# Kernel tuning notes

Hardware: AMD Instinct MI355X
Metric: run time of the kernel (lower is better)

Reference implementation:

```python
import jax, jax.numpy as jnp
import numpy as np

# dims derived from init_kwargs
B, C, T, F = 16, 2, 16, 256
TP, FP = 4, 4            # time/freq patch
MF = F // FP             # 64 freq tokens
TIC = T // TP            # 4 time tokens per chunk
S = MF * TIC             # 256 tokens per chunk
CTX = 3
LEFT = S * CTX           # 768 cached tokens
MT = TIC * (CTX + 1)     # 16 max time positions
D, H, G = 512, 8, 4      # d_model, q heads, kv groups
HD = D // H              # 64
R = H // G               # 2 q-heads per kv group
L = 4                    # layers
FFH = 4 * D
EPS = 1e-5


def _ln(x, g, b):
    m = jnp.mean(x, -1, keepdims=True)
    v = jnp.mean((x - m) ** 2, -1, keepdims=True)
    return (x - m) * jax.lax.rsqrt(v + EPS) * g + b


def setup_inputs() -> dict:
    key = jax.random.key(0)
    ks = iter(jax.random.split(key, 20))
    rn = lambda shape, s=0.05: jax.random.normal(next(ks), shape, jnp.float32) * s
    return {
        "x": rn((B, C, T, F), 1.0),
        "cache_k": rn((L, B, G, LEFT, HD), 1.0),
        "cache_v": rn((L, B, G, LEFT, HD), 1.0),
        "in_W": rn((TP * FP * C, D)), "in_b": jnp.zeros((D,)),
        "ln1_g": jnp.ones((L, D)), "ln1_b": jnp.zeros((L, D)),
        "Wq": rn((L, D, D)), "bq": jnp.zeros((L, D)),
        "Wk": rn((L, D, G * HD)), "bk": jnp.zeros((L, G * HD)),
        "Wv": rn((L, D, G * HD)), "bv": jnp.zeros((L, G * HD)),
        "Wo": rn((L, D, D)), "bo": jnp.zeros((L, D)),
        "rel_time": rn((L, 2 * MT - 1, H)), "rel_freq": rn((L, 2 * MF - 1, H)),
        "res_a": jnp.ones((L,)),
        "ln2_g": jnp.ones((L, D)), "ln2_b": jnp.zeros((L, D)),
        "W1": rn((L, D, FFH)), "b1": jnp.zeros((L, FFH)),
        "W3": rn((L, D, FFH)), "b3": jnp.zeros((L, FFH)),
        "W2": rn((L, FFH, D)), "b2": jnp.zeros((L, D)),
        "res_f": jnp.ones((L,)),
        "out_W": rn((D, TP * FP * C)), "out_b": jnp.zeros((TP * FP * C,)),
    }


def reference(x, cache_k, cache_v, in_W, in_b, ln1_g, ln1_b, Wq, bq, Wk, bk, Wv, bv,
              Wo, bo, rel_time, rel_freq, res_a, ln2_g, ln2_b, W1, b1, W3, b3, W2, b2,
              res_f, out_W, out_b):
    # patchify: (B,C,T,F) -> (B, S, TP*FP*C), token order time-major / freq inner
    h = jnp.transpose(x, (0, 2, 3, 1)).reshape(B, TIC, TP, MF, FP, C)
    h = jnp.transpose(h, (0, 1, 3, 2, 4, 5)).reshape(B, S, TP * FP * C)
    h = h @ in_W + in_b  # (B,S,D)

    # 2D relative position indices (identical each layer)
    K = LEFT + S
    q_idx = jnp.arange(S)
    k_idx = jnp.arange(K)
    qt = LEFT // MF + q_idx // MF  # query time = cache time offset + local time
    qf = q_idx % MF
    kt = k_idx // MF
    kf = k_idx % MF
    dt = qt[:, None] - kt[None, :] + (MT - 1)  # (S,K) in [0, 2*MT-2]
    df = qf[:, None] - kf[None, :] + (MF - 1)  # (S,K) in [0, 2*MF-2]
    scale = 1.0 / np.sqrt(HD).astype(np.float32)

    new_ck, new_cv = [], []
    for l in range(L):
        # --- streaming GQA attention with 2D rel-pos and KV cache ---
        xin = _ln(h, ln1_g[l], ln1_b[l])
        q = (xin @ Wq[l] + bq[l]).reshape(B, S, H, HD)
        k = (xin @ Wk[l] + bk[l]).reshape(B, S, G, HD)
        v = (xin @ Wv[l] + bv[l]).reshape(B, S, G, HD)
        k_full = jnp.concatenate([cache_k[l], jnp.transpose(k, (0, 2, 1, 3))], axis=2)  # (B,G,K,HD)
        v_full = jnp.concatenate([cache_v[l], jnp.transpose(v, (0, 2, 1, 3))], axis=2)
        new_ck.append(k_full[:, :, -LEFT:])
        new_cv.append(v_full[:, :, -LEFT:])
        # group q heads: head h -> group h // R
        scores = jnp.einsum('bsgrd,bgtd->bgrst', q.reshape(B, S, G, R, HD), k_full) * scale
        bias = rel_time[l][dt] + rel_freq[l][df]          # (S,K,H)
        bias = jnp.transpose(bias, (2, 0, 1)).reshape(G, R, S, K)
        attn = jax.nn.softmax(scores + bias[None], axis=-1)
        o = jnp.einsum('bgrst,bgtd->bsgrd', attn, v_full).reshape(B, S, D)
        o = o @ Wo[l] + bo[l]
        h = h + res_a[l] * o  # dropout/droppath identity at eval
        # --- SwiGLU FFN ---
        xin = _ln(h, ln2_g[l], ln2_b[l])
        ff = (jax.nn.silu(xin @ W1[l] + b1[l]) * (xin @ W3[l] + b3[l])) @ W2[l] + b2[l]
        h = h + res_f[l] * ff

    y = h @ out_W + out_b  # (B,S,TP*FP*C)
    # unpatchify back to (B,C,T,F)
    y = y.reshape(B, TIC, MF, TP, FP, C)
    y = jnp.transpose(y, (0, 1, 3, 2, 4, 5)).reshape(B, T, F, C)
    y = jnp.transpose(y, (0, 3, 1, 2))
    return y, jnp.stack(new_ck), jnp.stack(new_cv)
```

## Files before the change

kernel.cpp:

```cpp
#include <hip/hip_runtime.h>
#include <stdint.h>

typedef __attribute__((ext_vector_type(8))) short bf16x8;
typedef __attribute__((ext_vector_type(4))) float f32x4;

#define B_    16
#define S_    256
#define LEFT_ 768
#define KT_   1024
#define D_    512
#define H_    8
#define G_    4
#define HD_   64
#define L_    4
#define FFH_  2048
#define M_    4096

__device__ __forceinline__ unsigned short f2b(float f){
  unsigned u = __float_as_uint(f);
  u += 0x7fffu + ((u>>16)&1u);
  return (unsigned short)(u>>16);
}

__device__ __forceinline__ void gl_lds16(const unsigned short* g, void* l){
  __builtin_amdgcn_global_load_lds(
    (const __attribute__((address_space(1))) unsigned int*)g,
    (__attribute__((address_space(3))) unsigned int*)l, 16, 0, 0);
}

template<int BM, int BN, int WM, int WN, class BRowF>
__device__ __forceinline__ void mfma_core(
    const unsigned short* Abase, int lda, int m0, BRowF brow,
    int kd, char* As, char* Bs, f32x4* acc)
{
  constexpr int FR = WM/16, FC = WN/16;
  constexpr int NWC = BN/WN;
  constexpr int CA = BM/64, CB = BN/64;
  const int tid = threadIdx.x, wave = tid>>6, lane = tid&63;
  const int wr = wave / NWC, wc = wave % NWC;
  const int lr = lane>>2;
  const int swl = (lane&3) ^ ((lane>>2)&3) ^ (lane>>4);

  auto stage = [&](int buf, int k0){
    #pragma unroll
    for (int i = 0; i < CA; ++i) {
      const int chunk = wave*CA + i;
      const unsigned short* gp = Abase + (size_t)(m0 + chunk*16 + lr)*lda + k0 + swl*8;
      gl_lds16(gp, As + buf*(BM*64) + chunk*1024);
    }
    #pragma unroll
    for (int i = 0; i < CB; ++i) {
      const int chunk = wave*CB + i;
      const unsigned short* gp = brow(chunk*16 + lr) + k0 + swl*8;
      gl_lds16(gp, Bs + buf*(BN*64) + chunk*1024);
    }
  };

  stage(0, 0);
  __syncthreads();
  int cur = 0;
  for (int k0 = 0; k0 < kd; k0 += 32) {
    if (k0 + 32 < kd) stage(cur^1, k0 + 32);
    bf16x8 af[FR], bfr[FC];
    #pragma unroll
    for (int r = 0; r < FR; ++r)
      af[r] = *(const bf16x8*)(As + cur*(BM*64) + (wr*WM + r*16 + (lane&15))*64 + swl*16);
    #pragma unroll
    for (int c = 0; c < FC; ++c)
      bfr[c] = *(const bf16x8*)(Bs + cur*(BN*64) + (wc*WN + c*16 + (lane&15))*64 + swl*16);
    #pragma unroll
    for (int r = 0; r < FR; ++r)
      #pragma unroll
      for (int c = 0; c < FC; ++c)
        acc[r*FC+c] = __builtin_amdgcn_mfma_f32_16x16x32_bf16(af[r], bfr[c], acc[r*FC+c], 0, 0, 0);
    __syncthreads();
    cur ^= 1;
  }
}

__device__ __forceinline__ void tcvt_body(
    const float* __restrict__ src, unsigned short* __restrict__ dst,
    int K, int N, int ntk, int ntn, int bx)
{
  __shared__ float t[64][65];
  int kt = bx % ntk; int nt = (bx/ntk) % ntn; int l = bx/(ntk*ntn);
  src += (size_t)l*K*N; dst += (size_t)l*N*K;
  const int k0 = kt*64, n0 = nt*64;
  const int tid = threadIdx.x;
  #pragma unroll
  for (int i = 0; i < 4; ++i) {
    int kr = (tid>>4) + i*16;
    const float4 v = *(const float4*)&src[(size_t)(k0+kr)*N + n0 + (tid&15)*4];
    t[kr][(tid&15)*4+0]=v.x; t[kr][(tid&15)*4+1]=v.y;
    t[kr][(tid&15)*4+2]=v.z; t[kr][(tid&15)*4+3]=v.w;
  }
  __syncthreads();
  const int nn = tid>>2, kk = (tid&3)*16;
  unsigned w[8];
  #pragma unroll
  for (int j = 0; j < 8; ++j)
    w[j] = (unsigned)f2b(t[kk+2*j][nn]) | ((unsigned)f2b(t[kk+2*j+1][nn])<<16);
  size_t off = (size_t)(n0+nn)*K + k0 + kk;
  *(uint4*)&dst[off]     = make_uint4(w[0],w[1],w[2],w[3]);
  *(uint4*)&dst[off + 8] = make_uint4(w[4],w[5],w[6],w[7]);
}

__global__ __launch_bounds__(256) void transpose_all(
    const float* __restrict__ Wq, const float* __restrict__ Wk,
    const float* __restrict__ Wv, const float* __restrict__ Wo,
    const float* __restrict__ W1, const float* __restrict__ W3,
    const float* __restrict__ W2,
    unsigned short* __restrict__ Wqt, unsigned short* __restrict__ Wkt,
    unsigned short* __restrict__ Wvt, unsigned short* __restrict__ Wot,
    unsigned short* __restrict__ W1t, unsigned short* __restrict__ W3t,
    unsigned short* __restrict__ W2t)
{
  int bx = blockIdx.x;
  if      (bx < 256)  tcvt_body(Wq, Wqt, 512, 512, 8, 8,  bx);
  else if (bx < 384)  tcvt_body(Wk, Wkt, 512, 256, 8, 4,  bx-256);
  else if (bx < 512)  tcvt_body(Wv, Wvt, 512, 256, 8, 4,  bx-384);
  else if (bx < 768)  tcvt_body(Wo, Wot, 512, 512, 8, 8,  bx-512);
  else if (bx < 1792) tcvt_body(W1, W1t, 512, 2048, 8, 32, bx-768);
  else if (bx < 2816) tcvt_body(W3, W3t, 512, 2048, 8, 32, bx-1792);
  else                tcvt_body(W2, W2t, 2048, 512, 32, 8, bx-2816);
}

__global__ __launch_bounds__(256) void patchify_inproj(
    const float* __restrict__ x, const float* __restrict__ inW,
    const float* __restrict__ inb, float* __restrict__ h)
{
  int bs = blockIdx.x;
  int b = bs >> 8, s = bs & 255;
  int tic = s >> 6, mf = s & 63;
  __shared__ float ps[32];
  int tid = threadIdx.x;
  if (tid < 32) {
    int tp = tid >> 3, fp = (tid >> 1) & 3, c = tid & 1;
    ps[tid] = x[((size_t)(b*2 + c)*16 + tic*4 + tp)*256 + mf*4 + fp];
  }
  __syncthreads();
  #pragma unroll
  for (int rep = 0; rep < 2; ++rep) {
    int d = tid + rep*256;
    float acc = inb[d];
    #pragma unroll
    for (int i = 0; i < 32; ++i) acc += ps[i] * inW[i*D_ + d];
    h[(size_t)bs*D_ + d] = acc;
  }
}

__global__ __launch_bounds__(256) void ln_kernel(
    const float* __restrict__ in, unsigned short* __restrict__ out,
    const float* __restrict__ g, const float* __restrict__ bta)
{
  size_t row = blockIdx.x;
  const float* rp = in + row*D_;
  int tid = threadIdx.x;
  float x0 = rp[tid], x1 = rp[tid+256];
  float s = x0 + x1, sq = x0*x0 + x1*x1;
  __shared__ float red[10];
  #pragma unroll
  for (int o = 32; o > 0; o >>= 1) {
    s  += __shfl_down(s,  o, 64);
    sq += __shfl_down(sq, o, 64);
  }
  if ((tid & 63) == 0) { red[tid>>6] = s; red[4 + (tid>>6)] = sq; }
  __syncthreads();
  if (tid == 0) {
    float ts = red[0]+red[1]+red[2]+red[3];
    float tq = red[4]+red[5]+red[6]+red[7];
    float mean = ts * (1.0f/D_);
    float var  = tq * (1.0f/D_) - mean*mean;
    red[8] = mean; red[9] = 1.0f / sqrtf(var + 1e-5f);
  }
  __syncthreads();
  float mean = red[8], inv = red[9];
  unsigned short* op = out + row*D_;
  op[tid]     = f2b((x0-mean)*inv*g[tid]     + bta[tid]);
  op[tid+256] = f2b((x1-mean)*inv*g[tid+256] + bta[tid+256]);
}

__global__ __launch_bounds__(256) void qkv_ln_gemm(
    const float* __restrict__ h,
    const float* __restrict__ lng, const float* __restrict__ lnb,
    const unsigned short* __restrict__ Wqt, const unsigned short* __restrict__ Wkt,
    const unsigned short* __restrict__ Wvt,
    const float* __restrict__ bq, const float* __restrict__ bk_, const float* __restrict__ bv_,
    unsigned short* __restrict__ q_bf, unsigned short* __restrict__ kf_bf,
    unsigned short* __restrict__ vnew, float* __restrict__ nck, float* __restrict__ ncv)
{
  __shared__ alignas(16) char As[2][64*64];
  __shared__ alignas(16) char Bs[2][128*64];
  __shared__ float sm[64], sr[64];
  const int bx = blockIdx.x;
  const int mt = bx >> 3, nt = bx & 7;
  const int m0 = mt*64, n0 = nt*128;
  const int tid = threadIdx.x, wave = tid>>6, lane = tid&63;

  {
    const int r = tid >> 2, qd = tid & 3;
    const float* rp = h + (size_t)(m0 + r)*512 + qd*128;
    float s = 0.f, sq = 0.f;
    #pragma unroll
    for (int i = 0; i < 32; ++i) {
      float4 v = ((const float4*)rp)[i];
      s  += (v.x+v.y)+(v.z+v.w);
      sq += (v.x*v.x+v.y*v.y)+(v.z*v.z+v.w*v.w);
    }
    s += __shfl_xor(s,1,64); sq += __shfl_xor(sq,1,64);
    s += __shfl_xor(s,2,64); sq += __shfl_xor(sq,2,64);
    if (qd == 0) {
      float mean = s*(1.f/512.f);
      sm[r] = mean;
      sr[r] = rsqrtf(sq*(1.f/512.f) - mean*mean + 1e-5f);
    }
  }

  const int ar = tid >> 2, au = tid & 3;
  const int ap = au ^ (ar&3) ^ ((ar>>2)&3);
  const float* arow = h + (size_t)(m0 + ar)*512;

  const int lr = lane>>2;
  const int swl = (lane&3) ^ ((lane>>2)&3) ^ (lane>>4);
  auto brow = [&](int rr) -> const unsigned short* {
    int n = n0 + rr;
    return n < 512 ? Wqt + (size_t)n*512
         : n < 768 ? Wkt + (size_t)(n-512)*512
                   : Wvt + (size_t)(n-768)*512;
  };
  auto stageB = [&](int buf, int k0){
    #pragma unroll
    for (int i = 0; i < 2; ++i) {
      const int chunk = wave*2 + i;
      gl_lds16(brow(chunk*16+lr) + k0 + swl*8, (char*)Bs[buf] + chunk*1024);
    }
  };

  __syncthreads();
  const float mean_r = sm[ar], rstd_r = sr[ar];

  float4 av[6];
  auto loadA = [&](int k0){
    av[0] = *(const float4*)(arow + k0 + au*8);
    av[1] = *(const float4*)(arow + k0 + au*8 + 4);
    av[2] = *(const float4*)(lng  + k0 + au*8);
    av[3] = *(const float4*)(lng  + k0 + au*8 + 4);
    av[4] = *(const float4*)(lnb  + k0 + au*8);
    av[5] = *(const float4*)(lnb  + k0 + au*8 + 4);
  };
  auto writeA = [&](int buf){
    const float* xv = (const float*)&av[0];
    const float* gv = (const float*)&av[2];
    const float* bv2 = (const float*)&av[4];
    unsigned w[4];
    #pragma unroll
    for (int j = 0; j < 4; ++j) {
      float e0 = (xv[2*j]   - mean_r)*rstd_r*gv[2*j]   + bv2[2*j];
      float e1 = (xv[2*j+1] - mean_r)*rstd_r*gv[2*j+1] + bv2[2*j+1];
      w[j] = (unsigned)f2b(e0) | ((unsigned)f2b(e1)<<16);
    }
    *(uint4*)((char*)As[buf] + ar*64 + ap*16) = make_uint4(w[0],w[1],w[2],w[3]);
  };

  loadA(0);
  stageB(0, 0);
  writeA(0);
  __syncthreads();

  f32x4 acc[8] = {};
  const int wr = wave >> 1, wc = wave & 1;
  for (int k0 = 0; k0 < 512; k0 += 32) {
    const int cur = (k0>>5)&1;
    const bool more = (k0 + 32 < 512);
    if (more) { stageB(cur^1, k0+32); loadA(k0+32); }
    bf16x8 af[2], bfv[4];
    #pragma unroll
    for (int r = 0; r < 2; ++r)
      af[r] = *(const bf16x8*)((char*)As[cur] + (wr*32 + r*16 + (lane&15))*64 + swl*16);
    #pragma unroll
    for (int c = 0; c < 4; ++c)
      bfv[c] = *(const bf16x8*)((char*)Bs[cur] + (wc*64 + c*16 + (lane&15))*64 + swl*16);
    #pragma unroll
    for (int r = 0; r < 2; ++r)
      #pragma unroll
      for (int c = 0; c < 4; ++c)
        acc[r*4+c] = __builtin_amdgcn_mfma_f32_16x16x32_bf16(af[r], bfv[c], acc[r*4+c], 0,0,0);
    if (more) writeA(cur^1);
    __syncthreads();
  }

  #pragma unroll
  for (int r = 0; r < 2; ++r)
  #pragma unroll
  for (int c = 0; c < 4; ++c) {
    f32x4 v = acc[r*4+c];
    #pragma unroll
    for (int reg = 0; reg < 4; ++reg) {
      int m = m0 + wr*32 + r*16 + ((lane>>4)<<2) + reg;
      int n = n0 + wc*64 + c*16 + (lane&15);
      float val = v[reg];
      int b = m >> 8, s = m & 255;
      if (n < 512) {
        q_bf[(size_t)m*512 + n] = f2b(val + bq[n]);
      } else if (n < 768) {
        int g = (n-512) >> 6, hd = n & 63;
        float kv = val + bk_[n-512];
        kf_bf[((size_t)(b*4+g)*1024 + 768 + s)*64 + hd] = f2b(kv);
        nck [((size_t)(b*4+g)*768  + 512 + s)*64 + hd] = kv;
      } else {
        int g = (n-768) >> 6, hd = n & 63;
        float vv = val + bv_[n-768];
        vnew[(size_t)m*256 + (n-768)] = f2b(vv);
        ncv [((size_t)(b*4+g)*768 + 512 + s)*64 + hd] = vv;
      }
    }
  }
}

__global__ __launch_bounds__(256) void merge_kv(
    const float* __restrict__ ck, const float* __restrict__ cv,
    const unsigned short* __restrict__ vnew,
    unsigned short* __restrict__ kf_bf, unsigned short* __restrict__ vt_bf,
    float* __restrict__ nck, float* __restrict__ ncv)
{
  __shared__ float t[64][65];
  const int bb = blockIdx.x;
  const int tid = threadIdx.x;
  if (bb < 3072) {
    size_t idx = (size_t)bb*256 + tid;
    int hd4 = idx & 15;
    size_t tt = (idx >> 4) % 768;
    size_t bg = idx / (16*768);
    const float4 v = ((const float4*)ck)[idx];
    uint2 pk;
    pk.x = (unsigned)f2b(v.x) | ((unsigned)f2b(v.y)<<16);
    pk.y = (unsigned)f2b(v.z) | ((unsigned)f2b(v.w)<<16);
    *(uint2*)&kf_bf[((bg*1024 + tt)*64) + hd4*4] = pk;
    if (tt >= 256)
      ((float4*)nck)[(bg*768 + (tt-256))*16 + hd4] = v;
  } else if (bb < 3840) {
    const int bi = bb - 3072;
    const int bg = bi / 12, tt = bi % 12;
    const int t0 = tt*64;
    #pragma unroll
    for (int i = 0; i < 4; ++i) {
      int tr = (tid>>4) + i*16;
      const float4 v = ((const float4*)cv)[((size_t)bg*768 + t0+tr)*16 + (tid&15)];
      t[tr][(tid&15)*4+0]=v.x; t[tr][(tid&15)*4+1]=v.y;
      t[tr][(tid&15)*4+2]=v.z; t[tr][(tid&15)*4+3]=v.w;
      if (t0+tr >= 256)
        ((float4*)ncv)[((size_t)bg*768 + t0+tr-256)*16 + (tid&15)] = v;
    }
    __syncthreads();
    const int hd = tid>>2, tc = (tid&3)*16;
    unsigned w[8];
    #pragma unroll
    for (int j = 0; j < 8; ++j)
      w[j] = (unsigned)f2b(t[tc+2*j][hd]) | ((unsigned)f2b(t[tc+2*j+1][hd])<<16);
    size_t off = ((size_t)bg*64 + hd)*1024 + t0 + tc;
    *(uint4*)&vt_bf[off]     = make_uint4(w[0],w[1],w[2],w[3]);
    *(uint4*)&vt_bf[off + 8] = make_uint4(w[4],w[5],w[6],w[7]);
  } else {
    const int bi = bb - 3840;
    const int bg = bi >> 2, tt4 = bi & 3;
    const int b = bg >> 2, g = bg & 3;
    const int t0 = 768 + tt4*64;
    unsigned short* ts = (unsigned short*)&t[0][0];
    #pragma unroll
    for (int i = 0; i < 4; ++i) {
      int tr = (tid>>4) + i*16;
      uint2 v = *(const uint2*)&vnew[((size_t)(b*256 + (t0-768) + tr))*256 + g*64 + (tid&15)*4];
      const unsigned short* pv4 = (const unsigned short*)&v;
      ts[tr*68 + (tid&15)*4 + 0] = pv4[0];
      ts[tr*68 + (tid&15)*4 + 1] = pv4[1];
      ts[tr*68 + (tid&15)*4 + 2] = pv4[2];
      ts[tr*68 + (tid&15)*4 + 3] = pv4[3];
    }
    __syncthreads();
    const int hd = tid>>2, tc = (tid&3)*16;
    unsigned w[8];
    #pragma unroll
    for (int j = 0; j < 8; ++j)
      w[j] = (unsigned)ts[(tc+2*j)*68 + hd] | ((unsigned)ts[(tc+2*j+1)*68 + hd] << 16);
    size_t off = ((size_t)bg*64 + hd)*1024 + t0 + tc;
    *(uint4*)&vt_bf[off]     = make_uint4(w[0],w[1],w[2],w[3]);
    *(uint4*)&vt_bf[off + 8] = make_uint4(w[4],w[5],w[6],w[7]);
  }
}

__global__ __launch_bounds__(256) void flash_attn(
    const unsigned short* __restrict__ q_bf,
    const unsigned short* __restrict__ kf_bf,
    const unsigned short* __restrict__ vt_bf,
    const float* __restrict__ relt,
    const float* __restrict__ relf,
    unsigned short* __restrict__ att_bf)
{
  const int bx = blockIdx.x;
  const int qt = bx & 3, hh = (bx>>2) & 7, b = bx >> 5;
  const int g = hh >> 1;
  const int tid = threadIdx.x, wave = tid>>6, lane = tid&63;
  const int lg = lane>>4, lq = lane&15;
  const int q0 = qt*64;

  __shared__ alignas(16) char Ks[2][16384];
  __shared__ alignas(16) char Vs[2][16384];

  const unsigned short* kfb  = kf_bf + (size_t)(b*4+g)*1024*64;
  const unsigned short* vtb2 = vt_bf + (size_t)(b*4+g)*64*1024;

  auto stage = [&](int buf, int t){
    #pragma unroll
    for (int it = 0; it < 4; ++it) {
      int slot = it*256 + tid;
      int kr = slot>>3, kp = slot&7,  ku = kp ^ (kr&7);
      gl_lds16(kfb + (size_t)(t*128 + kr)*64 + ku*8, Ks[buf] + slot*16);
      int vr = slot>>4, vp = slot&15, vu = vp ^ (vr&15);
      gl_lds16(vtb2 + (size_t)vr*1024 + t*128 + vu*8, Vs[buf] + slot*16);
    }
  };

  const unsigned short* qrow = q_bf + ((size_t)(b*256 + q0 + wave*16 + lq))*512 + hh*64;
  bf16x8 qfrag[2];
  qfrag[0] = *(const bf16x8*)(qrow + lg*8);
  qfrag[1] = *(const bf16x8*)(qrow + 32 + lg*8);

  float bias_f[4][4];
  {
    int sq = wave*16 + lq;
    #pragma unroll
    for (int f = 0; f < 4; ++f)
      #pragma unroll
      for (int r = 0; r < 4; ++r)
        bias_f[f][r] = relf[((sq - (f*16 + lg*4 + r)) + 63)*8 + hh];
  }

  f32x4 ot[4] = {};
  float m_run = -1e30f, l_part = 0.f;

  stage(0, 0);
  __syncthreads();

  for (int t = 0; t < 8; ++t) {
    const int cur = t & 1;
    if (t + 1 < 8) stage(cur^1, t+1);

    f32x4 st[8] = {};
    #pragma unroll
    for (int c = 0; c < 2; ++c)
      #pragma unroll
      for (int f = 0; f < 8; ++f) {
        int row = f*16 + lq;
        int pu = (c*4 + lg) ^ (row & 7);
        bf16x8 kf_ = *(const bf16x8*)(Ks[cur] + row*128 + pu*16);
        st[f] = __builtin_amdgcn_mfma_f32_16x16x32_bf16(kf_, qfrag[c], st[f], 0,0,0);
      }

    const float bt0 = relt[(27 + qt - 2*t)*8 + hh];
    const float bt1 = relt[(27 + qt - 2*t - 1)*8 + hh];
    float mt = -1e30f;
    #pragma unroll
    for (int f = 0; f < 8; ++f) {
      const float bt = (f < 4) ? bt0 : bt1;
      #pragma unroll
      for (int r = 0; r < 4; ++r) {
        float v = st[f][r]*0.125f + bt + bias_f[f&3][r];
        st[f][r] = v;
        mt = fmaxf(mt, v);
      }
    }
    mt = fmaxf(mt, __shfl_xor(mt, 16, 64));
    mt = fmaxf(mt, __shfl_xor(mt, 32, 64));
    if (!__all(mt - m_run <= 8.0f)) {
      const float m_new = fmaxf(m_run, mt);
      const float corr = __expf(m_run - m_new);
      m_run = m_new;
      l_part *= corr;
      #pragma unroll
      for (int f = 0; f < 4; ++f) {
        ot[f][0] *= corr; ot[f][1] *= corr; ot[f][2] *= corr; ot[f][3] *= corr;
      }
    }
    float psum = 0.f;
    unsigned r01[8], r23[8];
    #pragma unroll
    for (int f = 0; f < 8; ++f) {
      float e0 = __expf(st[f][0] - m_run);
      float e1 = __expf(st[f][1] - m_run);
      float e2 = __expf(st[f][2] - m_run);
      float e3 = __expf(st[f][3] - m_run);
      psum += (e0+e1)+(e2+e3);
      r01[f] = (unsigned)f2b(e0) | ((unsigned)f2b(e1)<<16);
      r23[f] = (unsigned)f2b(e2) | ((unsigned)f2b(e3)<<16);
    }
    l_part += psum;

    const int src0 = (lg&1)*32 + lq;
    const int src1 = src0 + 16;
    const bool hi = (lg>>1) != 0;
    #pragma unroll
    for (int c = 0; c < 4; ++c) {
      unsigned a0 = (unsigned)__shfl((int)r01[c*2],   src0, 64);
      unsigned b0 = (unsigned)__shfl((int)r01[c*2+1], src0, 64);
      unsigned a1 = (unsigned)__shfl((int)r23[c*2],   src0, 64);
      unsigned b1 = (unsigned)__shfl((int)r23[c*2+1], src0, 64);
      unsigned a2 = (unsigned)__shfl((int)r01[c*2],   src1, 64);
      unsigned b2 = (unsigned)__shfl((int)r01[c*2+1], src1, 64);
      unsigned a3 = (unsigned)__shfl((int)r23[c*2],   src1, 64);
      unsigned b3 = (unsigned)__shfl((int)r23[c*2+1], src1, 64);
      uint4 bw;
      bw.x = hi ? b0 : a0;
      bw.y = hi ? b1 : a1;
      bw.z = hi ? b2 : a2;
      bw.w = hi ? b3 : a3;
      bf16x8 pfrag = *(bf16x8*)&bw;
      #pragma unroll
      for (int f = 0; f < 4; ++f) {
        int row = f*16 + lq;
        int pu = (c*4 + lg) ^ (row & 15);
        bf16x8 vf_ = *(const bf16x8*)(Vs[cur] + row*256 + pu*16);
        ot[f] = __builtin_amdgcn_mfma_f32_16x16x32_bf16(vf_, pfrag, ot[f], 0,0,0);
      }
    }
    __syncthreads();
  }

  float l_tot = l_part + __shfl_xor(l_part, 16, 64);
  l_tot += __shfl_xor(l_tot, 32, 64);
  const float inv = 1.0f / l_tot;
  unsigned short* orow = att_bf + ((size_t)(b*256 + q0 + wave*16 + lq))*512 + hh*64;
  #pragma unroll
  for (int f = 0; f < 4; ++f) {
    uint2 w;
    w.x = (unsigned)f2b(ot[f][0]*inv) | ((unsigned)f2b(ot[f][1]*inv)<<16);
    w.y = (unsigned)f2b(ot[f][2]*inv) | ((unsigned)f2b(ot[f][3]*inv)<<16);
    *(uint2*)(orow + f*16 + lg*4) = w;
  }
}

__global__ __launch_bounds__(256) void ffn1_gemm(
    const unsigned short* __restrict__ xin,
    const unsigned short* __restrict__ W1t, const unsigned short* __restrict__ W3t,
    const float* __restrict__ b1_, const float* __restrict__ b3_,
    unsigned short* __restrict__ ff_bf)
{
  __shared__ alignas(16) char As[2*128*64];
  __shared__ alignas(16) char Bs[2*128*64];
  f32x4 acc[16] = {};
  const int bx = blockIdx.x;
  const int nt = bx & 31, mt = bx >> 5;
  const int m0 = mt*128, n0 = nt*128;
  auto brow = [&](int r) -> const unsigned short* {
    int p = n0 + r;
    int pb = p >> 4;
    int j = ((pb>>1)<<4) | (p & 15);
    return (pb & 1) ? W3t + (size_t)j*512 : W1t + (size_t)j*512;
  };
  mfma_core<128,128,64,64>(xin, 512, m0, brow, 512, As, Bs, acc);
  const int lane = threadIdx.x & 63, wave = threadIdx.x >> 6;
  const int wr = wave >> 1, wc = wave & 1;
  #pragma unroll
  for (int r = 0; r < 4; ++r)
  #pragma unroll
  for (int cp = 0; cp < 4; cp += 2) {
    f32x4 va = acc[r*4+cp];
    f32x4 vb = acc[r*4+cp+1];
    #pragma unroll
    for (int reg = 0; reg < 4; ++reg) {
      int m = m0 + wr*64 + r*16 + ((lane>>4)<<2) + reg;
      int p = n0 + wc*64 + cp*16 + (lane&15);
      int j = ((p>>5)<<4) | (p & 15);
      float a = va[reg] + b1_[j];
      float bb = vb[reg] + b3_[j];
      float gval = (a / (1.0f + __expf(-a))) * bb;
      ff_bf[(size_t)m*2048 + j] = f2b(gval);
    }
  }
}

__global__ __launch_bounds__(256) void res_gemm(
    const unsigned short* __restrict__ A, int lda,
    const unsigned short* __restrict__ Wt, int kd,
    const float* __restrict__ bias, const float* __restrict__ resv,
    float* __restrict__ h)
{
  __shared__ alignas(16) char As[2*64*64];
  __shared__ alignas(16) char Bs[2*64*64];
  f32x4 acc[4] = {};
  const int bx = blockIdx.x;
  const int mt = bx >> 3, nt = bx & 7;
  const int m0 = mt*64, n0 = nt*64;
  auto brow = [&](int r) -> const unsigned short* {
    return Wt + (size_t)(n0 + r)*kd;
  };
  mfma_core<64,64,32,32>(A, lda, m0, brow, kd, As, Bs, acc);
  const float rv = resv[0];
  const int lane = threadIdx.x & 63, wave = threadIdx.x >> 6;
  const int wr = wave >> 1, wc = wave & 1;
  #pragma unroll
  for (int r = 0; r < 2; ++r)
  #pragma unroll
  for (int c = 0; c < 2; ++c) {
    f32x4 v = acc[r*2+c];
    #pragma unroll
    for (int reg = 0; reg < 4; ++reg) {
      int m = m0 + wr*32 + r*16 + ((lane>>4)<<2) + reg;
      int n = n0 + wc*32 + c*16 + (lane&15);
      h[(size_t)m*512 + n] += rv * (v[reg] + bias[n]);
    }
  }
}

__global__ __launch_bounds__(256) void outproj_kernel(
    const float* __restrict__ h, const float* __restrict__ outW,
    const float* __restrict__ outb, float* __restrict__ y)
{
  int bs = blockIdx.x;
  int b = bs >> 8, s = bs & 255;
  int tic = s >> 6, mf = s & 63;
  __shared__ float hr[512];
  __shared__ float part[8][32];
  int tid = threadIdx.x;
  hr[tid]     = h[(size_t)bs*D_ + tid];
  hr[tid+256] = h[(size_t)bs*D_ + tid + 256];
  __syncthreads();
  int i = tid & 31, seg = tid >> 5;
  float acc = 0.0f;
  #pragma unroll
  for (int k = 0; k < 64; ++k) acc += hr[seg*64 + k] * outW[(seg*64 + k)*32 + i];
  part[seg][i] = acc;
  __syncthreads();
  if (tid < 32) {
    float v = outb[tid];
    #pragma unroll
    for (int s2 = 0; s2 < 8; ++s2) v += part[s2][tid];
    int tp = tid >> 3, fp = (tid >> 1) & 3, c = tid & 1;
    y[((size_t)(b*2 + c)*16 + tic*4 + tp)*256 + mf*4 + fp] = v;
  }
}

extern "C" void kernel_launch(void* const* d_in, const int* in_sizes, int n_in,
                              void* d_out, int out_size, void* d_ws, size_t ws_size,
                              hipStream_t stream) {
  (void)in_sizes; (void)n_in; (void)out_size; (void)ws_size;
  const float* x        = (const float*)d_in[0];
  const float* cache_k  = (const float*)d_in[1];
  const float* cache_v  = (const float*)d_in[2];
  const float* in_W     = (const float*)d_in[3];
  const float* in_b     = (const float*)d_in[4];
  const float* ln1_g    = (const float*)d_in[5];
  const float* ln1_b    = (const float*)d_in[6];
  const float* Wq       = (const float*)d_in[7];
  const float* bq       = (const float*)d_in[8];
  const float* Wk       = (const float*)d_in[9];
  const float* bk       = (const float*)d_in[10];
  const float* Wv       = (const float*)d_in[11];
  const float* bv       = (const float*)d_in[12];
  const float* Wo       = (const float*)d_in[13];
  const float* bo       = (const float*)d_in[14];
  const float* rel_time = (const float*)d_in[15];
  const float* rel_freq = (const float*)d_in[16];
  const float* res_a    = (const float*)d_in[17];
  const float* ln2_g    = (const float*)d_in[18];
  const float* ln2_b    = (const float*)d_in[19];
  const float* W1       = (const float*)d_in[20];
  const float* b1       = (const float*)d_in[21];
  const float* W3       = (const float*)d_in[22];
  const float* b3       = (const float*)d_in[23];
  const float* W2       = (const float*)d_in[24];
  const float* b2       = (const float*)d_in[25];
  const float* res_f    = (const float*)d_in[26];
  const float* out_W    = (const float*)d_in[27];
  const float* out_b    = (const float*)d_in[28];

  char* ws = (char*)d_ws;
  size_t o = 0;
  float* h            = (float*)(ws + o);          o += (size_t)4096*512*4;
  unsigned short* xin = (unsigned short*)(ws + o); o += (size_t)4096*512*2;
  unsigned short* qb  = (unsigned short*)(ws + o); o += (size_t)4096*512*2;
  unsigned short* att = (unsigned short*)(ws + o); o += (size_t)4096*512*2;
  unsigned short* kfb = (unsigned short*)(ws + o); o += (size_t)64*1024*64*2;
  unsigned short* vtb = (unsigned short*)(ws + o); o += (size_t)64*64*1024*2;
  unsigned short* vnw = (unsigned short*)(ws + o); o += (size_t)4096*256*2;
  unsigned short* Wqt = (unsigned short*)(ws + o); o += (size_t)4*512*512*2;
  unsigned short* Wkt = (unsigned short*)(ws + o); o += (size_t)4*256*512*2;
  unsigned short* Wvt = (unsigned short*)(ws + o); o += (size_t)4*256*512*2;
  unsigned short* Wot = (unsigned short*)(ws + o); o += (size_t)4*512*512*2;
  unsigned short* W1t = (unsigned short*)(ws + o); o += (size_t)4*2048*512*2;
  unsigned short* W3t = (unsigned short*)(ws + o); o += (size_t)4*2048*512*2;
  unsigned short* W2t = (unsigned short*)(ws + o); o += (size_t)4*512*2048*2;
  unsigned short* ffb = (unsigned short*)(ws + o);

  float* y    = (float*)d_out;
  float* nck0 = y + 131072;
  float* ncv0 = nck0 + 12582912;

  transpose_all<<<3840, 256, 0, stream>>>(Wq, Wk, Wv, Wo, W1, W3, W2,
                                          Wqt, Wkt, Wvt, Wot, W1t, W3t, W2t);

  patchify_inproj<<<M_, 256, 0, stream>>>(x, in_W, in_b, h);

  for (int l = 0; l < L_; ++l) {
    qkv_ln_gemm<<<512, 256, 0, stream>>>(
        h, ln1_g + l*512, ln1_b + l*512,
        Wqt + (size_t)l*512*512, Wkt + (size_t)l*256*512, Wvt + (size_t)l*256*512,
        bq + l*512, bk + l*256, bv + l*256,
        qb, kfb, vnw, nck0 + (size_t)l*3145728, ncv0 + (size_t)l*3145728);
    merge_kv<<<4096, 256, 0, stream>>>(
        cache_k + (size_t)l*3145728, cache_v + (size_t)l*3145728, vnw,
        kfb, vtb, nck0 + (size_t)l*3145728, ncv0 + (size_t)l*3145728);
    flash_attn<<<512, 256, 0, stream>>>(qb, kfb, vtb,
        rel_time + l*31*8, rel_freq + l*127*8, att);
    res_gemm<<<512, 256, 0, stream>>>(att, 512, Wot + (size_t)l*512*512, 512,
                                      bo + l*512, res_a + l, h);
    ln_kernel<<<M_, 256, 0, stream>>>(h, xin, ln2_g + l*512, ln2_b + l*512);
    ffn1_gemm<<<1024, 256, 0, stream>>>(
        xin, W1t + (size_t)l*2048*512, W3t + (size_t)l*2048*512,
        b1 + l*2048, b3 + l*2048, ffb);
    res_gemm<<<512, 256, 0, stream>>>(ffb, 2048, W2t + (size_t)l*512*2048, 2048,
                                      b2 + l*512, res_f + l, h);
  }

  outproj_kernel<<<M_, 256, 0, stream>>>(h, out_W, out_b, y);
}
```

Before: 665.4 us.

## Precompute LN stats, remap block order for XCD locality, prioritise MFMA waves

Moves the layer-norm row statistics out of the QKV GEMM into a separate small kernel, so each of the eight N-tile blocks per row no longer recomputes the mean and variance over the full row. Remaps block indices in the QKV, attention and GEMM kernels so that blocks sharing the same A rows or KV head land on the same XCD, aiming for better L2 reuse. Raises wave priority around the MFMA loops in flash attention. The cost is an extra kernel launch per layer and a round trip for the statistics.

```diff
diff --git a/kernel.cpp b/kernel.cpp
--- a/kernel.cpp
+++ b/kernel.cpp
@@ -149,6 +149,29 @@
   }
 }
 
+__global__ __launch_bounds__(256) void ln_stats(
+    const float* __restrict__ h, float* __restrict__ smean, float* __restrict__ srstd)
+{
+  const int tid = threadIdx.x;
+  const int row = blockIdx.x*16 + (tid>>4);
+  const int qd = tid & 15;
+  const float* rp = h + (size_t)row*512 + qd*32;
+  float s = 0.f, sq = 0.f;
+  #pragma unroll
+  for (int i = 0; i < 8; ++i) {
+    float4 v = ((const float4*)rp)[i];
+    s  += (v.x+v.y)+(v.z+v.w);
+    sq += (v.x*v.x+v.y*v.y)+(v.z*v.z+v.w*v.w);
+  }
+  #pragma unroll
+  for (int o = 1; o < 16; o <<= 1) { s += __shfl_xor(s,o,64); sq += __shfl_xor(sq,o,64); }
+  if (qd == 0) {
+    float mean = s*(1.f/512.f);
+    smean[row] = mean;
+    srstd[row] = rsqrtf(sq*(1.f/512.f) - mean*mean + 1e-5f);
+  }
+}
+
 __global__ __launch_bounds__(256) void ln_kernel(
     const float* __restrict__ in, unsigned short* __restrict__ out,
     const float* __restrict__ g, const float* __restrict__ bta)
@@ -182,6 +205,7 @@
 
 __global__ __launch_bounds__(256) void qkv_ln_gemm(
     const float* __restrict__ h,
+    const float* __restrict__ smean, const float* __restrict__ srstd,
     const float* __restrict__ lng, const float* __restrict__ lnb,
     const unsigned short* __restrict__ Wqt, const unsigned short* __restrict__ Wkt,
     const unsigned short* __restrict__ Wvt,
@@ -191,34 +215,16 @@
 {
   __shared__ alignas(16) char As[2][64*64];
   __shared__ alignas(16) char Bs[2][128*64];
-  __shared__ float sm[64], sr[64];
-  const int bx = blockIdx.x;
+  int bx = (blockIdx.x & 7)*64 + (blockIdx.x >> 3);
   const int mt = bx >> 3, nt = bx & 7;
   const int m0 = mt*64, n0 = nt*128;
   const int tid = threadIdx.x, wave = tid>>6, lane = tid&63;
 
-  {
-    const int r = tid >> 2, qd = tid & 3;
-    const float* rp = h + (size_t)(m0 + r)*512 + qd*128;
-    float s = 0.f, sq = 0.f;
-    #pragma unroll
-    for (int i = 0; i < 32; ++i) {
-      float4 v = ((const float4*)rp)[i];
-      s  += (v.x+v.y)+(v.z+v.w);
-      sq += (v.x*v.x+v.y*v.y)+(v.z*v.z+v.w*v.w);
-    }
-    s += __shfl_xor(s,1,64); sq += __shfl_xor(sq,1,64);
-    s += __shfl_xor(s,2,64); sq += __shfl_xor(sq,2,64);
-    if (qd == 0) {
-      float mean = s*(1.f/512.f);
-      sm[r] = mean;
-      sr[r] = rsqrtf(sq*(1.f/512.f) - mean*mean + 1e-5f);
-    }
-  }
-
   const int ar = tid >> 2, au = tid & 3;
   const int ap = au ^ (ar&3) ^ ((ar>>2)&3);
   const float* arow = h + (size_t)(m0 + ar)*512;
+  const float mean_r = smean[m0 + ar];
+  const float rstd_r = srstd[m0 + ar];
 
   const int lr = lane>>2;
   const int swl = (lane&3) ^ ((lane>>2)&3) ^ (lane>>4);
@@ -235,9 +241,6 @@
       gl_lds16(brow(chunk*16+lr) + k0 + swl*8, (char*)Bs[buf] + chunk*1024);
     }
   };
-
-  __syncthreads();
-  const float mean_r = sm[ar], rstd_r = sr[ar];
 
   float4 av[6];
   auto loadA = [&](int k0){
@@ -396,7 +399,7 @@
     const float* __restrict__ relf,
     unsigned short* __restrict__ att_bf)
 {
-  const int bx = blockIdx.x;
+  int bx = (blockIdx.x & 7)*64 + (blockIdx.x >> 3);
   const int qt = bx & 3, hh = (bx>>2) & 7, b = bx >> 5;
   const int g = hh >> 1;
   const int tid = threadIdx.x, wave = tid>>6, lane = tid&63;
@@ -446,6 +449,7 @@
     if (t + 1 < 8) stage(cur^1, t+1);
 
     f32x4 st[8] = {};
+    __builtin_amdgcn_s_setprio(1);
     #pragma unroll
     for (int c = 0; c < 2; ++c)
       #pragma unroll
@@ -455,6 +459,7 @@
         bf16x8 kf_ = *(const bf16x8*)(Ks[cur] + row*128 + pu*16);
         st[f] = __builtin_amdgcn_mfma_f32_16x16x32_bf16(kf_, qfrag[c], st[f], 0,0,0);
       }
+    __builtin_amdgcn_s_setprio(0);
 
     const float bt0 = relt[(27 + qt - 2*t)*8 + hh];
     const float bt1 = relt[(27 + qt - 2*t - 1)*8 + hh];
@@ -514,6 +519,7 @@
       bw.z = hi ? b2 : a2;
       bw.w = hi ? b3 : a3;
       bf16x8 pfrag = *(bf16x8*)&bw;
+      __builtin_amdgcn_s_setprio(1);
       #pragma unroll
       for (int f = 0; f < 4; ++f) {
         int row = f*16 + lq;
@@ -521,6 +527,7 @@
         bf16x8 vf_ = *(const bf16x8*)(Vs[cur] + row*256 + pu*16);
         ot[f] = __builtin_amdgcn_mfma_f32_16x16x32_bf16(vf_, pfrag, ot[f], 0,0,0);
       }
+      __builtin_amdgcn_s_setprio(0);
     }
     __syncthreads();
   }
@@ -547,7 +554,7 @@
   __shared__ alignas(16) char As[2*128*64];
   __shared__ alignas(16) char Bs[2*128*64];
   f32x4 acc[16] = {};
-  const int bx = blockIdx.x;
+  int bx = (blockIdx.x & 7)*128 + (blockIdx.x >> 3);
   const int nt = bx & 31, mt = bx >> 5;
   const int m0 = mt*128, n0 = nt*128;
   auto brow = [&](int r) -> const unsigned short* {
@@ -587,7 +594,7 @@
   __shared__ alignas(16) char As[2*64*64];
   __shared__ alignas(16) char Bs[2*64*64];
   f32x4 acc[4] = {};
-  const int bx = blockIdx.x;
+  int bx = (blockIdx.x & 7)*64 + (blockIdx.x >> 3);
   const int mt = bx >> 3, nt = bx & 7;
   const int m0 = mt*64, n0 = nt*64;
   auto brow = [&](int r) -> const unsigned short* {
@@ -682,6 +689,8 @@
   unsigned short* kfb = (unsigned short*)(ws + o); o += (size_t)64*1024*64*2;
   unsigned short* vtb = (unsigned short*)(ws + o); o += (size_t)64*64*1024*2;
   unsigned short* vnw = (unsigned short*)(ws + o); o += (size_t)4096*256*2;
+  float* smean        = (float*)(ws + o);          o += (size_t)4096*4;
+  float* srstd        = (float*)(ws + o);          o += (size_t)4096*4;
   unsigned short* Wqt = (unsigned short*)(ws + o); o += (size_t)4*512*512*2;
   unsigned short* Wkt = (unsigned short*)(ws + o); o += (size_t)4*256*512*2;
   unsigned short* Wvt = (unsigned short*)(ws + o); o += (size_t)4*256*512*2;
@@ -701,8 +710,9 @@
   patchify_inproj<<<M_, 256, 0, stream>>>(x, in_W, in_b, h);
 
   for (int l = 0; l < L_; ++l) {
+    ln_stats<<<256, 256, 0, stream>>>(h, smean, srstd);
     qkv_ln_gemm<<<512, 256, 0, stream>>>(
-        h, ln1_g + l*512, ln1_b + l*512,
+        h, smean, srstd, ln1_g + l*512, ln1_b + l*512,
         Wqt + (size_t)l*512*512, Wkt + (size_t)l*256*512, Wvt + (size_t)l*256*512,
         bq + l*512, bk + l*256, bv + l*256,
         qb, kfb, vnw, nck0 + (size_t)l*3145728, ncv0 + (size_t)l*3145728);
```

Result: faster. 611.4 us (-8.1%).
